# Kernel tuning notes

Hardware: AMD Instinct MI355X
Metric: run time of the kernel (lower is better)

The kernel has to match this reference:

```python
import jax, jax.numpy as jnp
import numpy as np

NUM_HEAD = 16
MASKED_BIAS = -10000.0


def setup_inputs() -> dict:
    key = jax.random.key(0)
    k1, k2, k3 = jax.random.split(key, 3)
    B, M, N = 2, 2048, 1024
    x = jax.random.normal(k1, (B, M, N), dtype=jnp.float32)
    w_attn = jax.random.normal(k2, (N, 3 * N), dtype=jnp.float32) * 0.02
    w_proj = jax.random.normal(k3, (N, N), dtype=jnp.float32) * 0.02
    b_attn = jnp.zeros((3 * N,), dtype=jnp.float32)
    b_proj = jnp.zeros((N,), dtype=jnp.float32)
    return {"x": x, "w_attn": w_attn, "w_proj": w_proj,
            "b_attn": b_attn, "b_proj": b_proj}


def reference(x, w_attn, w_proj, b_attn, b_proj):
    B, M, N = x.shape
    H = NUM_HEAD
    d = N // H  # head dim
    # fused QKV projection: [B,M,3N]
    qkv = jnp.einsum('bmn,nd->bmd', x, w_attn) + b_attn
    q, k, v = jnp.split(qkv, 3, axis=-1)
    # split heads -> [B,H,M,d]
    q = q.reshape(B, M, H, d).transpose(0, 2, 1, 3)
    k = k.reshape(B, M, H, d).transpose(0, 2, 1, 3)
    v = v.reshape(B, M, H, d).transpose(0, 2, 1, 3)
    # scaled dot-product scores [B,H,M,M]
    scores = jnp.einsum('bhqd,bhkd->bhqk', q, k) / jnp.sqrt(jnp.float32(d))
    causal = jnp.tril(jnp.ones((M, M), dtype=bool))  # GPT-2 bias buffer
    scores = jnp.where(causal, scores, jnp.float32(MASKED_BIAS))
    attn = jax.nn.softmax(scores, axis=-1)
    # context [B,H,M,d] -> [B,M,N]
    ctx = jnp.einsum('bhqk,bhkd->bhqd', attn, v)
    ctx = ctx.transpose(0, 2, 1, 3).reshape(B, M, N)
    # output projection
    out = jnp.einsum('bmn,no->bmo', ctx, w_proj) + b_proj
    return out
```

## Files before the change

kernel.cpp:

```cpp
#include <hip/hip_runtime.h>

typedef __attribute__((ext_vector_type(8))) __bf16 bf16x8;
typedef __attribute__((ext_vector_type(4))) float f32x4;

__device__ __forceinline__ void async_copy16(const void* g, void* l) {
    __builtin_amdgcn_global_load_lds(
        (const __attribute__((address_space(1))) void*)g,
        (__attribute__((address_space(3))) void*)l, 16, 0, 0);
}

__global__ __launch_bounds__(256) void cast_bf16_k(
    const float* __restrict__ src, __bf16* __restrict__ dst)
{
    size_t i = ((size_t)blockIdx.x * 256 + threadIdx.x) * 8;
    float4 a = *(const float4*)&src[i];
    float4 b = *(const float4*)&src[i + 4];
    bf16x8 o;
    o[0] = (__bf16)a.x; o[1] = (__bf16)a.y; o[2] = (__bf16)a.z; o[3] = (__bf16)a.w;
    o[4] = (__bf16)b.x; o[5] = (__bf16)b.y; o[6] = (__bf16)b.z; o[7] = (__bf16)b.w;
    *(bf16x8*)&dst[i] = o;
}

__global__ __launch_bounds__(256) void transpose_cast_k(
    const float* __restrict__ src, __bf16* __restrict__ dst, int R, int C)
{
    __shared__ float tile[32][33];
    int c0 = blockIdx.x * 32, r0 = blockIdx.y * 32;
    int tx = threadIdx.x & 31, ty = threadIdx.x >> 5;
    for (int i = ty; i < 32; i += 8)
        tile[i][tx] = src[(size_t)(r0 + i) * C + (c0 + tx)];
    __syncthreads();
    for (int i = ty; i < 32; i += 8)
        dst[(size_t)(c0 + i) * R + (r0 + tx)] = (__bf16)tile[tx][i];
}

template <int MODE>
__global__ __launch_bounds__(256) void gemm_bt(
    const __bf16* __restrict__ A, const __bf16* __restrict__ Bt,
    const float* __restrict__ bias, int K,
    __bf16* __restrict__ O0, __bf16* __restrict__ O1, __bf16* __restrict__ O2,
    float* __restrict__ Of)
{
    __shared__ __align__(16) __bf16 lds_a[128 * 32];
    __shared__ __align__(16) __bf16 lds_b[128 * 32];
    const int row0 = blockIdx.x * 128;
    const int col0 = blockIdx.y * 128;
    const int tid  = threadIdx.x;
    const int lane = tid & 63;
    const int w    = tid >> 6;
    const int wm   = (w >> 1) * 64, wn = (w & 1) * 64;
    const int quad = lane >> 4, l16 = lane & 15;
    const int rsw  = (quad ^ (l16 & 3)) * 8;

    f32x4 acc[4][4] = {};
    for (int kb = 0; kb < K; kb += 32) {
#pragma unroll
        for (int t = 0; t < 2; ++t) {
            int c = t * 64 + lane;
            int row = 32 * w + (c >> 2);
            int gch = (c & 3) ^ (row & 3);
            async_copy16(&A[(size_t)(row0 + row) * K + kb + gch * 8],
                         (char*)lds_a + (w * 128 + t * 64) * 16);
            async_copy16(&Bt[(size_t)(col0 + row) * K + kb + gch * 8],
                         (char*)lds_b + (w * 128 + t * 64) * 16);
        }
        __syncthreads();
        bf16x8 af[4], bfr[4];
#pragma unroll
        for (int i = 0; i < 4; ++i)
            af[i] = *(const bf16x8*)&lds_a[(wm + i * 16 + l16) * 32 + rsw];
#pragma unroll
        for (int j = 0; j < 4; ++j)
            bfr[j] = *(const bf16x8*)&lds_b[(wn + j * 16 + l16) * 32 + rsw];
#pragma unroll
        for (int i = 0; i < 4; ++i)
#pragma unroll
            for (int j = 0; j < 4; ++j)
                acc[i][j] = __builtin_amdgcn_mfma_f32_16x16x32_bf16(
                    af[i], bfr[j], acc[i][j], 0, 0, 0);
        __syncthreads();
    }

#pragma unroll
    for (int i = 0; i < 4; ++i) {
        int grow = row0 + wm + i * 16 + quad * 4;
#pragma unroll
        for (int j = 0; j < 4; ++j) {
            int gcol = col0 + wn + j * 16 + l16;
            float bv = bias[gcol];
            if constexpr (MODE == 0) {
                int which = gcol >> 10;
                int n  = gcol & 1023;
                int hh = n >> 6, dd = n & 63;
#pragma unroll
                for (int r = 0; r < 4; ++r) {
                    int gr = grow + r;
                    int bb = gr >> 11, mm = gr & 2047;
                    int bhh = bb * 16 + hh;
                    float v = acc[i][j][r] + bv;
                    if (which == 0)
                        O0[((size_t)bhh * 2048 + mm) * 64 + dd] =
                            (__bf16)(v * 0.125f);
                    else if (which == 1)
                        O1[((size_t)bhh * 2048 + mm) * 64 + dd] = (__bf16)v;
                    else
                        O2[((size_t)bhh * 64 + dd) * 2048 + mm] = (__bf16)v;
                }
            } else {
#pragma unroll
                for (int r = 0; r < 4; ++r) {
                    int gr = grow + r;
                    Of[(size_t)gr * 1024 + gcol] = acc[i][j][r] + bv;
                }
            }
        }
    }
}

__global__ __launch_bounds__(256) void attn_kernel(
    const __bf16* __restrict__ Qh, const __bf16* __restrict__ Kh,
    const __bf16* __restrict__ Vt, __bf16* __restrict__ ctx)
{
    const int M = 2048, D = 64;
    const int g = blockIdx.x, h = blockIdx.y, b = blockIdx.z;
    const int bh = b * 16 + h;
    const int tid = threadIdx.x, lane = tid & 63, w = tid >> 6;
    const int quad = lane >> 4, l16 = lane & 15;

    const int qA = g * 64, qB = (31 - g) * 64;
    const int nIter = 32 - g;

    __shared__ __align__(16) __bf16 lds_k[2][64 * 64];
    __shared__ __align__(16) __bf16 lds_v[2][64 * 64];
    __shared__ __align__(16) __bf16 lds_p[4][16 * 72];

    const __bf16* Qp = Qh + (size_t)bh * M * D;
    const __bf16* Kp = Kh + (size_t)bh * M * D;
    const __bf16* Vp = Vt + (size_t)bh * D * M;

    const int qb0[2] = { qA + w * 16, qB + w * 16 };

    bf16x8 qf[2][2];
#pragma unroll
    for (int reg = 0; reg < 2; ++reg)
#pragma unroll
        for (int c = 0; c < 2; ++c)
            qf[reg][c] = *(const bf16x8*)
                &Qp[(size_t)(qb0[reg] + l16) * D + c * 32 + quad * 8];

    f32x4 acc[2][4] = {};
    float lrow[2][4] = {};

    auto stage = [&](int pb, int kb) {
#pragma unroll
        for (int t = 0; t < 2; ++t) {
            int c = w * 128 + t * 64 + lane;
            int row = c >> 3, ch = c & 7;
            int gch = ch ^ (row & 7);
            async_copy16(&Kp[(size_t)(kb + row) * 64 + gch * 8],
                         (char*)&lds_k[pb][0] + (w * 128 + t * 64) * 16);
            async_copy16(&Vp[(size_t)row * M + kb + gch * 8],
                         (char*)&lds_v[pb][0] + (w * 128 + t * 64) * 16);
        }
    };

    stage(0, 0);
    __bf16* pl = &lds_p[w][0];

    for (int it = 0; it < nIter; ++it) {
        const int kb = it << 6;
        __syncthreads();
        if (it + 1 < nIter) stage((it + 1) & 1, kb + 64);
        const __bf16* kt = &lds_k[it & 1][0];
        const __bf16* vt = &lds_v[it & 1][0];

#pragma unroll
        for (int reg = 0; reg < 2; ++reg) {
            const int qbase = qb0[reg];
            if (kb > qbase + 15) continue;

            f32x4 s[4];
#pragma unroll
            for (int j = 0; j < 4; ++j) {
                f32x4 t = {};
#pragma unroll
                for (int c = 0; c < 2; ++c) {
                    int ch = ((c << 2) + quad) ^ (l16 & 7);
                    bf16x8 kf = *(const bf16x8*)
                        &kt[(((j << 4) + l16) << 6) + (ch << 3)];
                    t = __builtin_amdgcn_mfma_f32_16x16x32_bf16(
                        qf[reg][c], kf, t, 0, 0, 0);
                }
                s[j] = t;
            }
            if (kb + 63 > qbase) {
#pragma unroll
                for (int j = 0; j < 4; ++j)
#pragma unroll
                    for (int r = 0; r < 4; ++r)
                        if (kb + j * 16 + l16 > qbase + quad * 4 + r)
                            s[j][r] = -1e30f;
            }
#pragma unroll
            for (int r = 0; r < 4; ++r) {
                float rs = 0.f;
#pragma unroll
                for (int j = 0; j < 4; ++j) {
                    float p = __expf(s[j][r]);
                    s[j][r] = p;
                    rs += p;
                }
                rs += __shfl_xor(rs, 1);
                rs += __shfl_xor(rs, 2);
                rs += __shfl_xor(rs, 4);
                rs += __shfl_xor(rs, 8);
                lrow[reg][r] += rs;
            }
#pragma unroll
            for (int j = 0; j < 4; ++j)
#pragma unroll
                for (int r = 0; r < 4; ++r)
                    pl[(quad * 4 + r) * 72 + j * 16 + l16] = (__bf16)s[j][r];
            bf16x8 pf[2];
#pragma unroll
            for (int c = 0; c < 2; ++c)
                pf[c] = *(const bf16x8*)&pl[l16 * 72 + c * 32 + quad * 8];
#pragma unroll
            for (int f = 0; f < 4; ++f)
#pragma unroll
                for (int c = 0; c < 2; ++c) {
                    int ch = ((c << 2) + quad) ^ (l16 & 7);
                    bf16x8 vf = *(const bf16x8*)
                        &vt[(((f << 4) + l16) << 6) + (ch << 3)];
                    acc[reg][f] = __builtin_amdgcn_mfma_f32_16x16x32_bf16(
                        pf[c], vf, acc[reg][f], 0, 0, 0);
                }
        }
    }

#pragma unroll
    for (int reg = 0; reg < 2; ++reg)
#pragma unroll
        for (int f = 0; f < 4; ++f)
#pragma unroll
            for (int r = 0; r < 4; ++r) {
                int q = qb0[reg] + quad * 4 + r;
                int col = h * 64 + f * 16 + l16;
                ctx[((size_t)(b * 2048 + q)) * 1024 + col] =
                    (__bf16)(acc[reg][f][r] / lrow[reg][r]);
            }
}

extern "C" void kernel_launch(void* const* d_in, const int* in_sizes, int n_in,
                              void* d_out, int out_size, void* d_ws, size_t ws_size,
                              hipStream_t stream) {
    const float* x      = (const float*)d_in[0];
    const float* w_attn = (const float*)d_in[1];
    const float* w_proj = (const float*)d_in[2];
    const float* b_attn = (const float*)d_in[3];
    const float* b_proj = (const float*)d_in[4];
    float* out = (float*)d_out;

    char* ws = (char*)d_ws;
    __bf16* xb  = (__bf16*)(ws);
    __bf16* ctx = (__bf16*)(ws);
    __bf16* wAt = (__bf16*)(ws + 8388608);
    __bf16* wPt = (__bf16*)(ws + 14680064);
    __bf16* Vt  = (__bf16*)(ws + 16777216);
    __bf16* Qh  = (__bf16*)d_out;
    __bf16* Kh  = (__bf16*)d_out + 4194304;

    cast_bf16_k<<<2048, 256, 0, stream>>>(x, xb);
    transpose_cast_k<<<dim3(96, 32), 256, 0, stream>>>(w_attn, wAt, 1024, 3072);
    transpose_cast_k<<<dim3(32, 32), 256, 0, stream>>>(w_proj, wPt, 1024, 1024);
    gemm_bt<0><<<dim3(32, 24), 256, 0, stream>>>(xb, wAt, b_attn, 1024,
                                                 Qh, Kh, Vt, nullptr);
    attn_kernel<<<dim3(16, 16, 2), 256, 0, stream>>>(Qh, Kh, Vt, ctx);
    gemm_bt<1><<<dim3(32, 8), 256, 0, stream>>>(ctx, wPt, b_proj, 1024,
                                                nullptr, nullptr, nullptr, out);
}
```

Before: 214.0 us.

## Compute softmax row sums via MFMA, use exp2, coalesce V-transpose epilogue

The attention kernel now gets softmax denominators by multiplying the bf16 P tile with a ones vector on the matrix cores, which replaces the per-row shuffle reductions. It also folds log2(e) into the Q scale so it can call exp2f. The QKV GEMM epilogue for the V section now transposes the tile through LDS and writes 16-byte coalesced rows into the transposed V layout, instead of scattered 2-byte stores. The trade-offs are extra MFMA work, row sums taken from bf16-rounded probabilities, and extra LDS traffic and barriers in the epilogue.

```diff
diff --git a/kernel.cpp b/kernel.cpp
--- a/kernel.cpp
+++ b/kernel.cpp
@@ -1,6 +1,7 @@
 #include <hip/hip_runtime.h>
 
 typedef __attribute__((ext_vector_type(8))) __bf16 bf16x8;
+typedef __attribute__((ext_vector_type(4))) __bf16 bf16x4;
 typedef __attribute__((ext_vector_type(4))) float f32x4;
 
 __device__ __forceinline__ void async_copy16(const void* g, void* l) {
@@ -41,8 +42,9 @@
     __bf16* __restrict__ O0, __bf16* __restrict__ O1, __bf16* __restrict__ O2,
     float* __restrict__ Of)
 {
-    __shared__ __align__(16) __bf16 lds_a[128 * 32];
-    __shared__ __align__(16) __bf16 lds_b[128 * 32];
+    __shared__ __align__(16) __bf16 smem[8704];
+    __bf16* lds_a = smem;
+    __bf16* lds_b = smem + 4096;
     const int row0 = blockIdx.x * 128;
     const int col0 = blockIdx.y * 128;
     const int tid  = threadIdx.x;
@@ -81,14 +83,54 @@
         __syncthreads();
     }
 
-#pragma unroll
-    for (int i = 0; i < 4; ++i) {
-        int grow = row0 + wm + i * 16 + quad * 4;
-#pragma unroll
-        for (int j = 0; j < 4; ++j) {
-            int gcol = col0 + wn + j * 16 + l16;
-            float bv = bias[gcol];
-            if constexpr (MODE == 0) {
+    if constexpr (MODE == 0) {
+        if (col0 >= 2048) {
+            __bf16* ldsT = smem;
+            const int bb  = row0 >> 11;
+            const int mm0 = row0 & 2047;
+#pragma unroll
+            for (int half = 0; half < 2; ++half) {
+                if ((wn >> 6) == half) {
+#pragma unroll
+                    for (int j = 0; j < 4; ++j) {
+                        int nl = (wn & 63) + j * 16 + l16;
+                        float bv = bias[col0 + wn + j * 16 + l16];
+#pragma unroll
+                        for (int i = 0; i < 4; ++i) {
+                            int mrow = wm + i * 16 + quad * 4;
+                            bf16x4 pk;
+#pragma unroll
+                            for (int r = 0; r < 4; ++r)
+                                pk[r] = (__bf16)(acc[i][j][r] + bv);
+                            *(bf16x4*)&ldsT[nl * 136 + mrow] = pk;
+                        }
+                    }
+                }
+                __syncthreads();
+                {
+                    int nl = tid >> 2;
+                    int gcol = col0 + half * 64 + nl;
+                    int nn = gcol & 1023;
+                    int hh = nn >> 6, dd = nn & 63;
+                    int bhh = bb * 16 + hh;
+                    __bf16* dstrow = &O2[((size_t)bhh * 64 + dd) * 2048 + mm0];
+#pragma unroll
+                    for (int c8 = 0; c8 < 4; ++c8) {
+                        int m = (tid & 3) * 32 + c8 * 8;
+                        *(bf16x8*)&dstrow[m] = *(const bf16x8*)&ldsT[nl * 136 + m];
+                    }
+                }
+                __syncthreads();
+            }
+            return;
+        }
+#pragma unroll
+        for (int i = 0; i < 4; ++i) {
+            int grow = row0 + wm + i * 16 + quad * 4;
+#pragma unroll
+            for (int j = 0; j < 4; ++j) {
+                int gcol = col0 + wn + j * 16 + l16;
+                float bv = bias[gcol];
                 int which = gcol >> 10;
                 int n  = gcol & 1023;
                 int hh = n >> 6, dd = n & 63;
@@ -100,13 +142,20 @@
                     float v = acc[i][j][r] + bv;
                     if (which == 0)
                         O0[((size_t)bhh * 2048 + mm) * 64 + dd] =
-                            (__bf16)(v * 0.125f);
-                    else if (which == 1)
+                            (__bf16)(v * 0.18033688011112042f);
+                    else
                         O1[((size_t)bhh * 2048 + mm) * 64 + dd] = (__bf16)v;
-                    else
-                        O2[((size_t)bhh * 64 + dd) * 2048 + mm] = (__bf16)v;
-                }
-            } else {
+                }
+            }
+        }
+    } else {
+#pragma unroll
+        for (int i = 0; i < 4; ++i) {
+            int grow = row0 + wm + i * 16 + quad * 4;
+#pragma unroll
+            for (int j = 0; j < 4; ++j) {
+                int gcol = col0 + wn + j * 16 + l16;
+                float bv = bias[gcol];
 #pragma unroll
                 for (int r = 0; r < 4; ++r) {
                     int gr = grow + r;
@@ -149,7 +198,9 @@
                 &Qp[(size_t)(qb0[reg] + l16) * D + c * 32 + quad * 8];
 
     f32x4 acc[2][4] = {};
-    float lrow[2][4] = {};
+    f32x4 acc_s[2] = {};
+    const __bf16 onev = (__bf16)1.0f;
+    const bf16x8 ones = {onev, onev, onev, onev, onev, onev, onev, onev};
 
     auto stage = [&](int pb, int kb) {
 #pragma unroll
@@ -202,20 +253,10 @@
                             s[j][r] = -1e30f;
             }
 #pragma unroll
-            for (int r = 0; r < 4; ++r) {
-                float rs = 0.f;
-#pragma unroll
-                for (int j = 0; j < 4; ++j) {
-                    float p = __expf(s[j][r]);
-                    s[j][r] = p;
-                    rs += p;
-                }
-                rs += __shfl_xor(rs, 1);
-                rs += __shfl_xor(rs, 2);
-                rs += __shfl_xor(rs, 4);
-                rs += __shfl_xor(rs, 8);
-                lrow[reg][r] += rs;
-            }
+            for (int j = 0; j < 4; ++j)
+#pragma unroll
+                for (int r = 0; r < 4; ++r)
+                    s[j][r] = exp2f(s[j][r]);
 #pragma unroll
             for (int j = 0; j < 4; ++j)
 #pragma unroll
@@ -235,6 +276,10 @@
                     acc[reg][f] = __builtin_amdgcn_mfma_f32_16x16x32_bf16(
                         pf[c], vf, acc[reg][f], 0, 0, 0);
                 }
+#pragma unroll
+            for (int c = 0; c < 2; ++c)
+                acc_s[reg] = __builtin_amdgcn_mfma_f32_16x16x32_bf16(
+                    pf[c], ones, acc_s[reg], 0, 0, 0);
         }
     }
 
@@ -247,7 +292,7 @@
                 int q = qb0[reg] + quad * 4 + r;
                 int col = h * 64 + f * 16 + l16;
                 ctx[((size_t)(b * 2048 + q)) * 1024 + col] =
-                    (__bf16)(acc[reg][f][r] / lrow[reg][r]);
+                    (__bf16)(acc[reg][f][r] / acc_s[reg][r]);
             }
 }
 
```

Measured after the change: 220.0 us. 2.8% more time.

## Split attention into per-tile blocks, use exp2 softmax and MFMA row sums

Applied to the files above, without the earlier changes.

Each attention block now processes one 64-row query tile instead of a paired short and long tile. The grid becomes 32x32, with heads on x and query tiles reversed on y so the longest tiles launch first. The log2(e) factor is folded into the Q scaling so the kernel can call exp2f directly. Row sums now come from an MFMA against a ones vector rather than shuffle reductions, which removes per-row shuffles but rounds P to bf16 before summing and doubles the number of blocks, each reloading K/V tiles.

```diff
diff --git a/kernel.cpp b/kernel.cpp
--- a/kernel.cpp
+++ b/kernel.cpp
@@ -100,7 +100,7 @@
                     float v = acc[i][j][r] + bv;
                     if (which == 0)
                         O0[((size_t)bhh * 2048 + mm) * 64 + dd] =
-                            (__bf16)(v * 0.125f);
+                            (__bf16)(v * 0.18033688011112042f);
                     else if (which == 1)
                         O1[((size_t)bhh * 2048 + mm) * 64 + dd] = (__bf16)v;
                     else
@@ -122,13 +122,14 @@
     const __bf16* __restrict__ Vt, __bf16* __restrict__ ctx)
 {
     const int M = 2048, D = 64;
-    const int g = blockIdx.x, h = blockIdx.y, b = blockIdx.z;
-    const int bh = b * 16 + h;
+    const int bh = blockIdx.x;
+    const int qt = 31 - blockIdx.y;
+    const int b = bh >> 4, h = bh & 15;
     const int tid = threadIdx.x, lane = tid & 63, w = tid >> 6;
     const int quad = lane >> 4, l16 = lane & 15;
 
-    const int qA = g * 64, qB = (31 - g) * 64;
-    const int nIter = 32 - g;
+    const int q0 = qt * 64;
+    const int nIter = qt + 1;
 
     __shared__ __align__(16) __bf16 lds_k[2][64 * 64];
     __shared__ __align__(16) __bf16 lds_v[2][64 * 64];
@@ -138,18 +139,18 @@
     const __bf16* Kp = Kh + (size_t)bh * M * D;
     const __bf16* Vp = Vt + (size_t)bh * D * M;
 
-    const int qb0[2] = { qA + w * 16, qB + w * 16 };
-
-    bf16x8 qf[2][2];
-#pragma unroll
-    for (int reg = 0; reg < 2; ++reg)
-#pragma unroll
-        for (int c = 0; c < 2; ++c)
-            qf[reg][c] = *(const bf16x8*)
-                &Qp[(size_t)(qb0[reg] + l16) * D + c * 32 + quad * 8];
-
-    f32x4 acc[2][4] = {};
-    float lrow[2][4] = {};
+    const int qbase = q0 + w * 16;
+
+    bf16x8 qf[2];
+#pragma unroll
+    for (int c = 0; c < 2; ++c)
+        qf[c] = *(const bf16x8*)
+            &Qp[(size_t)(qbase + l16) * D + c * 32 + quad * 8];
+
+    f32x4 acc[4] = {};
+    f32x4 acc_s = {};
+    const __bf16 onev = (__bf16)1.0f;
+    const bf16x8 ones = {onev, onev, onev, onev, onev, onev, onev, onev};
 
     auto stage = [&](int pb, int kb) {
 #pragma unroll
@@ -174,81 +175,67 @@
         const __bf16* kt = &lds_k[it & 1][0];
         const __bf16* vt = &lds_v[it & 1][0];
 
-#pragma unroll
-        for (int reg = 0; reg < 2; ++reg) {
-            const int qbase = qb0[reg];
-            if (kb > qbase + 15) continue;
-
-            f32x4 s[4];
-#pragma unroll
-            for (int j = 0; j < 4; ++j) {
-                f32x4 t = {};
-#pragma unroll
-                for (int c = 0; c < 2; ++c) {
-                    int ch = ((c << 2) + quad) ^ (l16 & 7);
-                    bf16x8 kf = *(const bf16x8*)
-                        &kt[(((j << 4) + l16) << 6) + (ch << 3)];
-                    t = __builtin_amdgcn_mfma_f32_16x16x32_bf16(
-                        qf[reg][c], kf, t, 0, 0, 0);
-                }
-                s[j] = t;
+        f32x4 s[4];
+#pragma unroll
+        for (int j = 0; j < 4; ++j) {
+            f32x4 t = {};
+#pragma unroll
+            for (int c = 0; c < 2; ++c) {
+                int ch = ((c << 2) + quad) ^ (l16 & 7);
+                bf16x8 kf = *(const bf16x8*)
+                    &kt[(((j << 4) + l16) << 6) + (ch << 3)];
+                t = __builtin_amdgcn_mfma_f32_16x16x32_bf16(
+                    qf[c], kf, t, 0, 0, 0);
             }
-            if (kb + 63 > qbase) {
-#pragma unroll
-                for (int j = 0; j < 4; ++j)
-#pragma unroll
-                    for (int r = 0; r < 4; ++r)
-                        if (kb + j * 16 + l16 > qbase + quad * 4 + r)
-                            s[j][r] = -1e30f;
+            s[j] = t;
+        }
+        if (kb + 63 > qbase) {
+#pragma unroll
+            for (int j = 0; j < 4; ++j)
+#pragma unroll
+                for (int r = 0; r < 4; ++r)
+                    if (kb + j * 16 + l16 > qbase + quad * 4 + r)
+                        s[j][r] = -1e30f;
+        }
+#pragma unroll
+        for (int j = 0; j < 4; ++j)
+#pragma unroll
+            for (int r = 0; r < 4; ++r)
+                s[j][r] = exp2f(s[j][r]);
+#pragma unroll
+        for (int j = 0; j < 4; ++j)
+#pragma unroll
+            for (int r = 0; r < 4; ++r)
+                pl[(quad * 4 + r) * 72 + j * 16 + l16] = (__bf16)s[j][r];
+        bf16x8 pf[2];
+#pragma unroll
+        for (int c = 0; c < 2; ++c)
+            pf[c] = *(const bf16x8*)&pl[l16 * 72 + c * 32 + quad * 8];
+#pragma unroll
+        for (int f = 0; f < 4; ++f)
+#pragma unroll
+            for (int c = 0; c < 2; ++c) {
+                int ch = ((c << 2) + quad) ^ (l16 & 7);
+                bf16x8 vf = *(const bf16x8*)
+                    &vt[(((f << 4) + l16) << 6) + (ch << 3)];
+                acc[f] = __builtin_amdgcn_mfma_f32_16x16x32_bf16(
+                    pf[c], vf, acc[f], 0, 0, 0);
             }
 #pragma unroll
-            for (int r = 0; r < 4; ++r) {
-                float rs = 0.f;
-#pragma unroll
-                for (int j = 0; j < 4; ++j) {
-                    float p = __expf(s[j][r]);
-                    s[j][r] = p;
-                    rs += p;
-                }
-                rs += __shfl_xor(rs, 1);
-                rs += __shfl_xor(rs, 2);
-                rs += __shfl_xor(rs, 4);
-                rs += __shfl_xor(rs, 8);
-                lrow[reg][r] += rs;
-            }
-#pragma unroll
-            for (int j = 0; j < 4; ++j)
-#pragma unroll
-                for (int r = 0; r < 4; ++r)
-                    pl[(quad * 4 + r) * 72 + j * 16 + l16] = (__bf16)s[j][r];
-            bf16x8 pf[2];
-#pragma unroll
-            for (int c = 0; c < 2; ++c)
-                pf[c] = *(const bf16x8*)&pl[l16 * 72 + c * 32 + quad * 8];
-#pragma unroll
-            for (int f = 0; f < 4; ++f)
-#pragma unroll
-                for (int c = 0; c < 2; ++c) {
-                    int ch = ((c << 2) + quad) ^ (l16 & 7);
-                    bf16x8 vf = *(const bf16x8*)
-                        &vt[(((f << 4) + l16) << 6) + (ch << 3)];
-                    acc[reg][f] = __builtin_amdgcn_mfma_f32_16x16x32_bf16(
-                        pf[c], vf, acc[reg][f], 0, 0, 0);
-                }
-        }
+        for (int c = 0; c < 2; ++c)
+            acc_s = __builtin_amdgcn_mfma_f32_16x16x32_bf16(
+                pf[c], ones, acc_s, 0, 0, 0);
     }
 
 #pragma unroll
-    for (int reg = 0; reg < 2; ++reg)
-#pragma unroll
-        for (int f = 0; f < 4; ++f)
-#pragma unroll
-            for (int r = 0; r < 4; ++r) {
-                int q = qb0[reg] + quad * 4 + r;
-                int col = h * 64 + f * 16 + l16;
-                ctx[((size_t)(b * 2048 + q)) * 1024 + col] =
-                    (__bf16)(acc[reg][f][r] / lrow[reg][r]);
-            }
+    for (int f = 0; f < 4; ++f)
+#pragma unroll
+        for (int r = 0; r < 4; ++r) {
+            int q = qbase + quad * 4 + r;
+            int col = h * 64 + f * 16 + l16;
+            ctx[((size_t)(b * 2048 + q)) * 1024 + col] =
+                (__bf16)(acc[f][r] / acc_s[r]);
+        }
 }
 
 extern "C" void kernel_launch(void* const* d_in, const int* in_sizes, int n_in,
@@ -275,7 +262,7 @@
     transpose_cast_k<<<dim3(32, 32), 256, 0, stream>>>(w_proj, wPt, 1024, 1024);
     gemm_bt<0><<<dim3(32, 24), 256, 0, stream>>>(xb, wAt, b_attn, 1024,
                                                  Qh, Kh, Vt, nullptr);
-    attn_kernel<<<dim3(16, 16, 2), 256, 0, stream>>>(Qh, Kh, Vt, ctx);
+    attn_kernel<<<dim3(32, 32), 256, 0, stream>>>(Qh, Kh, Vt, ctx);
     gemm_bt<1><<<dim3(32, 8), 256, 0, stream>>>(ctx, wPt, b_proj, 1024,
                                                 nullptr, nullptr, nullptr, out);
 }
```

New measurement: 201.3 us. 1.06x faster.
